# Kernel optimization log

Measured on AMD Instinct MI355X. Metric: run time of the kernel, lower is better.

## Reference

```python
import jax, jax.numpy as jnp
import numpy as np

D_MODEL = 512
NUM_HEADS = 8
D_K = D_MODEL // NUM_HEADS
SCALE = 1.0 / np.sqrt(D_K).astype(np.float32)


def _relative_shift(x):
    # x: (B, H, S, P) pos scores from Q @ P^T; Transformer-XL shift trick.
    b, h, s, p = x.shape
    x = jnp.pad(x, ((0, 0), (0, 0), (0, 0), (1, 0)))   # (B,H,S,P+1)
    x = x.reshape(b, h, p + 1, s)[:, :, 1:, :]          # drop first row
    x = x.reshape(b, h, s, p)[:, :, :, :s]
    return x


def setup_inputs() -> dict:
    key = jax.random.key(0)
    ks = jax.random.split(key, 10)
    B, S = 4, 2048
    glorot = lambda k: jax.random.uniform(
        k, (D_MODEL, D_MODEL), jnp.float32,
        -np.sqrt(6.0 / (2 * D_MODEL)), np.sqrt(6.0 / (2 * D_MODEL)))
    return {
        "inputs": jax.random.normal(ks[0], (B, S, D_MODEL), jnp.float32),
        "pos_enc": jax.random.normal(ks[1], (1, S, D_MODEL), jnp.float32),
        "W_q": glorot(ks[2]),
        "W_k": glorot(ks[3]),
        "W_v": glorot(ks[4]),
        "W_o": glorot(ks[5]),
        "W_pos": glorot(ks[6]),
        "u_bias": jnp.zeros((NUM_HEADS, D_K), jnp.float32),
        "v_bias": jnp.zeros((NUM_HEADS, D_K), jnp.float32),
    }


def reference(inputs, pos_enc, W_q, W_k, W_v, W_o, W_pos, u_bias, v_bias):
    B, S, _ = inputs.shape
    split = lambda x, b: x.reshape(b, S, NUM_HEADS, D_K).transpose(0, 2, 1, 3)
    Q = split(inputs @ W_q, B)        # (B,H,S,dk)
    K = split(inputs @ W_k, B)
    V = split(inputs @ W_v, B)
    P = split(pos_enc @ W_pos, 1)      # (1,H,S,dk)
    u = u_bias[None, :, None, :]
    v = v_bias[None, :, None, :]
    content_score = jnp.einsum('bhid,bhjd->bhij', Q + u, K)
    pos_score = jnp.einsum('bhid,xhjd->bhij', Q + v, P)  # broadcast over batch
    pos_score = _relative_shift(pos_score)
    scores = (content_score + pos_score) * SCALE
    attn = jax.nn.softmax(scores, axis=-1)  # no dropout (inference)
    context = jnp.einsum('bhij,bhjd->bhid', attn, V)
    context = context.transpose(0, 2, 1, 3).reshape(B, S, D_MODEL)
    return context @ W_o
```

## Files before the change

kernel.cpp:

```cpp
#include <hip/hip_runtime.h>
#include <hip/hip_bf16.h>
#include <math.h>

#define SEQ 2048
#define NH 8
#define DK 64
#define DM 512
#define QSCALE 0.18033688011112042f
#define PPAD (SEQ + 128)
#define POFF 64
#define KSTR 72
#define PSTR 36
#define ASTR 34

typedef unsigned short ushortT;
typedef short s16x8 __attribute__((ext_vector_type(8)));
typedef float f32x4 __attribute__((ext_vector_type(4)));

#define MFMA16 __builtin_amdgcn_mfma_f32_16x16x32_bf16

static __device__ __forceinline__ ushortT f2bf(float x) {
  __hip_bfloat16 h = __float2bfloat16(x);
  ushortT u;
  __builtin_memcpy(&u, &h, 2);
  return u;
}

static __device__ __forceinline__ float fexp2(float x) {
  return __builtin_amdgcn_exp2f(x);
}

static __device__ __forceinline__ s16x8 pack8(const float* p) {
  ushortT u[8];
#pragma unroll
  for (int i = 0; i < 8; ++i) u[i] = f2bf(p[i]);
  s16x8 out;
  __builtin_memcpy(&out, u, 16);
  return out;
}

static __device__ __forceinline__ int pinv(int j) {
  return (j < 16) ? ((j >> 2) * 8 + (j & 3)) : (((j >> 2) - 4) * 8 + 4 + (j & 3));
}

__global__ __launch_bounds__(256)
void cast_in(const float* __restrict__ X, const float* __restrict__ PE,
             ushortT* __restrict__ Xb, ushortT* __restrict__ PEb) {
  const size_t i4 = (size_t)blockIdx.x * 256 + threadIdx.x;
  const size_t NX = (size_t)4 * SEQ * DM / 4;
  const float4 v = (i4 < NX) ? *(const float4*)(X + i4 * 4)
                             : *(const float4*)(PE + (i4 - NX) * 4);
  ushortT o[4] = {f2bf(v.x), f2bf(v.y), f2bf(v.z), f2bf(v.w)};
  ushortT* dst = (i4 < NX) ? (Xb + i4 * 4) : (PEb + (i4 - NX) * 4);
  *(ulonglong1*)dst = *(ulonglong1*)o;
}

__global__ __launch_bounds__(256)
void transpose_w(const float* __restrict__ w0, const float* __restrict__ w1,
                 const float* __restrict__ w2, const float* __restrict__ w3,
                 const float* __restrict__ w4, ushortT* __restrict__ out) {
  __shared__ float ts[32][33];
  const int z = blockIdx.z;
  const float* w = (z == 0) ? w0 : (z == 1) ? w1 : (z == 2) ? w2 : (z == 3) ? w3 : w4;
  ushortT* o = out + (size_t)z * DM * DM;
  const int k0 = blockIdx.x * 32, n0 = blockIdx.y * 32;
  const int tx = threadIdx.x, ty = threadIdx.y;
#pragma unroll
  for (int i = 0; i < 4; ++i)
    ts[ty + i * 8][tx] = w[(size_t)(k0 + ty + i * 8) * DM + n0 + tx];
  __syncthreads();
#pragma unroll
  for (int i = 0; i < 4; ++i)
    o[(size_t)(n0 + ty + i * 8) * DM + k0 + tx] = f2bf(ts[tx][ty + i * 8]);
}

__global__ __launch_bounds__(256)
void gemm_mfma(const ushortT* __restrict__ A, const ushortT* __restrict__ Bt,
               const float* __restrict__ ubv, const float* __restrict__ vbv,
               ushortT* __restrict__ qu, ushortT* __restrict__ qv,
               ushortT* __restrict__ kb, ushortT* __restrict__ vt,
               float* __restrict__ of, int mode) {
  __shared__ ushortT As[128][ASTR];
  __shared__ ushortT Bs[128][ASTR];
  const int tid = threadIdx.x;
  const int w = tid >> 6, lane = tid & 63;
  const int c = lane & 15, q = lane >> 4;
  const int wm = w >> 1, wn = w & 1;
  const int m0 = blockIdx.x * 128, n0 = blockIdx.y * 128;
  const int lr = tid >> 1, lh = (tid & 1) * 16;

  f32x4 acc[4][4];
#pragma unroll
  for (int mt = 0; mt < 4; ++mt)
#pragma unroll
    for (int nt = 0; nt < 4; ++nt) acc[mt][nt] = (f32x4){0.f, 0.f, 0.f, 0.f};

  const ushortT* Ar = A + (size_t)(m0 + lr) * DM + lh;
  const ushortT* Br = Bt + (size_t)(n0 + lr) * DM + lh;
  uint4 a0 = *(const uint4*)(Ar);
  uint4 a1 = *(const uint4*)(Ar + 8);
  uint4 b0 = *(const uint4*)(Br);
  uint4 b1 = *(const uint4*)(Br + 8);

  for (int k0 = 0; k0 < DM; k0 += 32) {
    __syncthreads();
    *(uint4*)&As[lr][lh] = a0; *(uint4*)&As[lr][lh + 8] = a1;
    *(uint4*)&Bs[lr][lh] = b0; *(uint4*)&Bs[lr][lh + 8] = b1;
    __syncthreads();
    if (k0 + 32 < DM) {
      a0 = *(const uint4*)(Ar + k0 + 32);
      a1 = *(const uint4*)(Ar + k0 + 40);
      b0 = *(const uint4*)(Br + k0 + 32);
      b1 = *(const uint4*)(Br + k0 + 40);
    }
    s16x8 af[4], bf[4];
#pragma unroll
    for (int mt = 0; mt < 4; ++mt)
      af[mt] = *(const s16x8*)&As[wm * 64 + mt * 16 + c][q * 8];
#pragma unroll
    for (int nt = 0; nt < 4; ++nt)
      bf[nt] = *(const s16x8*)&Bs[wn * 64 + nt * 16 + c][q * 8];
#pragma unroll
    for (int mt = 0; mt < 4; ++mt)
#pragma unroll
      for (int nt = 0; nt < 4; ++nt)
        acc[mt][nt] = MFMA16(af[mt], bf[nt], acc[mt][nt], 0, 0, 0);
  }

#pragma unroll
  for (int mt = 0; mt < 4; ++mt)
#pragma unroll
    for (int nt = 0; nt < 4; ++nt)
#pragma unroll
      for (int r = 0; r < 4; ++r) {
        const int gm = m0 + wm * 64 + mt * 16 + q * 4 + r;
        const int gn = n0 + wn * 64 + nt * 16 + c;
        const float v = acc[mt][nt][r];
        const int bb = gm >> 11, s = gm & (SEQ - 1);
        if (mode == 0) {
          const int z = gn >> 9, gn5 = gn & 511;
          const int h = gn5 >> 6, d = gn5 & 63;
          if (z == 0) {
            const size_t base = (((size_t)bb * NH + h) * SEQ + s) * DK + d;
            qu[base] = f2bf((v + ubv[gn5]) * QSCALE);
            qv[base] = f2bf((v + vbv[gn5]) * QSCALE);
          } else if (z == 1) {
            kb[(((size_t)bb * NH + h) * SEQ + s) * DK + d] = f2bf(v);
          } else {
            const int s_il = (s & ~31) | pinv(s & 31);
            vt[(((size_t)bb * NH + h) * DK + d) * SEQ + s_il] = f2bf(v);
          }
        } else if (mode == 3) {
          const int h = gn >> 6, d = gn & 63;
          qu[((size_t)h * PPAD + POFF + gm) * DK + d] = f2bf(v);
        } else {
          of[(size_t)gm * DM + gn] = v;
        }
      }
}

static __device__ __forceinline__ f32x4 band_gemm(const ushortT* pb, int tile,
                                                  int c, int q, s16x8 a0, s16x8 a1) {
  const ushortT* pc = pb + (ptrdiff_t)(tile * 16 + c) * DK + q * 8;
  f32x4 G = {0.f, 0.f, 0.f, 0.f};
  G = MFMA16(a0, *(const s16x8*)pc, G, 0, 0, 0);
  G = MFMA16(a1, *(const s16x8*)(pc + 32), G, 0, 0, 0);
  return G;
}

static __device__ __forceinline__ f32x4 band_gemm_r(s16x8 a0, s16x8 a1,
                                                    s16x8 p0, s16x8 p1) {
  f32x4 G = {0.f, 0.f, 0.f, 0.f};
  G = MFMA16(a0, p0, G, 0, 0, 0);
  G = MFMA16(a1, p1, G, 0, 0, 0);
  return G;
}

static __device__ __forceinline__ void write_band2(float (*E)[PSTR], int c, int m_w,
                                                   f32x4 b0, f32x4 b1, f32x4 b2) {
#pragma unroll
  for (int r = 0; r < 4; ++r) {
    const int v = c + m_w + r - 15;
    const bool lo = (v >= 0);
    const int j1 = lo ? v : v + 16;
    const int p = ((j1 >> 2) << 3) | (j1 & 3);
    float* row = &E[m_w + r][p];
    row[0] = lo ? b0[r] : b1[r];
    row[4] = lo ? b1[r] : b2[r];
  }
}

__global__ __launch_bounds__(256, 3)
void attn_mfma(const ushortT* __restrict__ Qu, const ushortT* __restrict__ Qv,
               const ushortT* __restrict__ Kb, const ushortT* __restrict__ Vt,
               const ushortT* __restrict__ Pp, ushortT* __restrict__ ctxb) {
  const int n = blockIdx.x;
  const int xcd = n & 7, idx = n >> 3;
  const int b = idx >> 5, iblk = idx & 31;
  const int h = xcd, bh = b * 8 + h;
  const int tid = threadIdx.x;
  const int w = tid >> 6, lane = tid & 63;
  const int c = lane & 15, q = lane >> 4;
  const int i0 = iblk * 64;
  const int iw = i0 + w * 16;

  __shared__ ushortT Ks[64][KSTR];
  __shared__ ushortT Vs[64][KSTR];
  __shared__ float E1[4][2][16][PSTR];
  __shared__ float Lb[4][16];

  const ushortT* Qub = Qu + ((size_t)bh * SEQ + iw) * DK;
  const ushortT* Qvb = Qv + ((size_t)bh * SEQ + iw) * DK;
  const ushortT* Kbh = Kb + (size_t)bh * SEQ * DK;
  const ushortT* Vbh = Vt + (size_t)bh * DK * SEQ;
  const ushortT* Ph  = Pp + ((size_t)h * PPAD + POFF) * DK;

  const s16x8 qu0 = *(const s16x8*)(Qub + (size_t)c * DK + q * 8);
  const s16x8 qu1 = *(const s16x8*)(Qub + (size_t)c * DK + 32 + q * 8);
  const s16x8 qv0 = *(const s16x8*)(Qvb + (size_t)c * DK + q * 8);
  const s16x8 qv1 = *(const s16x8*)(Qvb + (size_t)c * DK + 32 + q * 8);
  const s16x8 qw0 = *(const s16x8*)(Qvb + (size_t)(c + 1) * DK + q * 8);
  const s16x8 qw1 = *(const s16x8*)(Qvb + (size_t)(c + 1) * DK + 32 + q * 8);

  int joff[8];
#pragma unroll
  for (int jj = 0; jj < 8; ++jj)
    joff[jj] = (jj < 4) ? (4 * q + jj) : (16 + 4 * q + (jj - 4));

  f32x4 O[4];
#pragma unroll
  for (int r = 0; r < 4; ++r) O[r] = (f32x4){0.f, 0.f, 0.f, 0.f};
  float lrow = 0.f;
  f32x4 e2c = (f32x4){0.f, 0.f, 0.f, 0.f};
  bool hv1 = false, hv2 = false;
  const int jt = iw & ~31;
  const int m_w = q * 4;

  {
    const ushortT* gk = Kbh;
    uint4 k0v = *(const uint4*)(gk + tid * 8);
    uint4 k1v = *(const uint4*)(gk + 2048 + tid * 8);
    const ushortT* gv = Vbh + (size_t)(tid >> 2) * SEQ + (tid & 3) * 16;
    uint4 v0v = *(const uint4*)gv;
    uint4 v1v = *(const uint4*)(gv + 8);
    *(uint4*)&Ks[tid >> 3][(tid & 7) * 8] = k0v;
    *(uint4*)&Ks[32 + (tid >> 3)][(tid & 7) * 8] = k1v;
    *(uint4*)&Vs[tid >> 2][(tid & 3) * 16] = v0v;
    *(uint4*)&Vs[tid >> 2][(tid & 3) * 16 + 8] = v1v;
  }
  __syncthreads();

  if (jt > 0) {
    const ushortT* pb1 = Ph + (ptrdiff_t)(0 - iw + SEQ - 16) * DK;
    f32x4 b0 = band_gemm(pb1, 0, c, q, qv0, qv1);
    f32x4 b1 = band_gemm(pb1, 1, c, q, qv0, qv1);
    e2c = band_gemm(pb1, 2, c, q, qv0, qv1);
    hv1 = true;
    write_band2(E1[w][0], c, m_w, b0, b1, e2c);
  }

#define PV_FROM(pr, jl)                                                       \
  {                                                                           \
    lrow += pr[0] + pr[1] + pr[2] + pr[3] + pr[4] + pr[5] + pr[6] + pr[7];    \
    const s16x8 pa = pack8(pr);                                               \
    _Pragma("unroll")                                                         \
    for (int dt = 0; dt < 4; ++dt) {                                          \
      const s16x8 vb = *(const s16x8*)&Vs[dt * 16 + c][(jl) + q * 8];         \
      O[dt] = MFMA16(pa, vb, O[dt], 0, 0, 0);                                 \
    }                                                                         \
  }

  for (int ch = 0; ch < 32; ++ch) {
    const bool more = (ch + 1) < 32;
    uint4 k0v, k1v, v0v, v1v;
    if (more) {
      const ushortT* gk = Kbh + (size_t)(ch + 1) * 64 * DK;
      k0v = *(const uint4*)(gk + tid * 8);
      k1v = *(const uint4*)(gk + 2048 + tid * 8);
      const ushortT* gv = Vbh + (size_t)(tid >> 2) * SEQ + (ch + 1) * 64 + (tid & 3) * 16;
      v0v = *(const uint4*)gv;
      v1v = *(const uint4*)(gv + 8);
    }
#pragma unroll
    for (int t = 0; t < 2; ++t) {
      const int nn = ch * 2 + t;
      const int j0 = nn * 32;
      const int jl = t * 32;
      const int drel = j0 - iw;
      const bool curB = (j0 >= jt) && (j0 < jt + 64);
      const int j0n = j0 + 32;
      const bool nxtB = (j0n >= jt) && (j0n < jt + 64);
      const bool haveNext = (nn + 1 < 64) && !nxtB;
      const bool nextA = (j0n < jt);

      const int dreln = j0n - iw;
      const int row1 = haveNext ? (nextA ? (dreln + SEQ - 16) : (dreln - 17)) : 0;
      const ushortT* pbn = Ph + (ptrdiff_t)row1 * DK;
      const ushortT* pc1 = pbn + (ptrdiff_t)(16 + c) * DK + q * 8;
      const ushortT* pc2 = pbn + (ptrdiff_t)(32 + c) * DK + q * 8;
      const s16x8 p10 = *(const s16x8*)pc1;
      const s16x8 p11 = *(const s16x8*)(pc1 + 32);
      const s16x8 p20 = *(const s16x8*)pc2;
      const s16x8 p21 = *(const s16x8*)(pc2 + 32);

      f32x4 S0 = {0.f, 0.f, 0.f, 0.f}, S1 = {0.f, 0.f, 0.f, 0.f};
      {
        const ushortT* ka = &Ks[jl + c][q * 8];
        S0 = MFMA16(*(const s16x8*)ka, qu0, S0, 0, 0, 0);
        S0 = MFMA16(*(const s16x8*)(ka + 32), qu1, S0, 0, 0, 0);
        const ushortT* ka2 = &Ks[jl + 16 + c][q * 8];
        S1 = MFMA16(*(const s16x8*)ka2, qu0, S1, 0, 0, 0);
        S1 = MFMA16(*(const s16x8*)(ka2 + 32), qu1, S1, 0, 0, 0);
      }

      if (curB) {
        {
          const ushortT* pb1 = Ph + (ptrdiff_t)(drel + SEQ - 16) * DK;
          f32x4 b0 = band_gemm(pb1, 0, c, q, qv0, qv1);
          f32x4 b1 = band_gemm(pb1, 1, c, q, qv0, qv1);
          f32x4 b2 = band_gemm(pb1, 2, c, q, qv0, qv1);
          write_band2(E1[w][nn & 1], c, m_w, b0, b1, b2);
        }
        {
          const ushortT* pb2 = Ph + (ptrdiff_t)(drel - 17) * DK;
          f32x4 b0 = band_gemm(pb2, 0, c, q, qw0, qw1);
          f32x4 b1 = band_gemm(pb2, 1, c, q, qw0, qw1);
          f32x4 b2 = band_gemm(pb2, 2, c, q, qw0, qw1);
          write_band2(E1[w][(nn + 1) & 1], c, m_w, b0, b1, b2);
        }
        const float* e1r = &E1[w][nn & 1][c][q * 8];
        const float* e2r = &E1[w][(nn + 1) & 1][c][q * 8];
        float4 aA = *(const float4*)e1r, aB = *(const float4*)(e1r + 4);
        float4 bA = *(const float4*)e2r, bB = *(const float4*)(e2r + 4);
        float f1[8] = {aA.x, aA.y, aA.z, aA.w, aB.x, aB.y, aB.z, aB.w};
        float f2[8] = {bA.x, bA.y, bA.z, bA.w, bB.x, bB.y, bB.z, bB.w};
        float sv[8] = {S0[0], S0[1], S0[2], S0[3], S1[0], S1[1], S1[2], S1[3]};
        float pr[8];
#pragma unroll
        for (int jj = 0; jj < 8; ++jj) {
          const int dlt = drel + joff[jj] - c;
          const float g = (dlt <= 0) ? f1[jj] : ((dlt == 1) ? 0.0f : f2[jj]);
          pr[jj] = fexp2(sv[jj] + g);
        }
        PV_FROM(pr, jl)
      } else {
        const float* e1r = &E1[w][nn & 1][c][q * 8];
        float4 fA = *(const float4*)e1r, fB = *(const float4*)(e1r + 4);
        float pr[8] = {fexp2(S0[0] + fA.x), fexp2(S0[1] + fA.y),
                       fexp2(S0[2] + fA.z), fexp2(S0[3] + fA.w),
                       fexp2(S1[0] + fB.x), fexp2(S1[1] + fB.y),
                       fexp2(S1[2] + fB.z), fexp2(S1[3] + fB.w)};
        PV_FROM(pr, jl)
      }

      if (haveNext) {
        f32x4 b0, b1, b2;
        if (nextA) {
          if (hv1) b0 = e2c;
          else { b0 = band_gemm(pbn, 0, c, q, qv0, qv1); hv1 = true; }
          b1 = band_gemm_r(qv0, qv1, p10, p11);
          b2 = band_gemm_r(qv0, qv1, p20, p21);
        } else {
          if (hv2) b0 = e2c;
          else { b0 = band_gemm(pbn, 0, c, q, qw0, qw1); hv2 = true; }
          b1 = band_gemm_r(qw0, qw1, p10, p11);
          b2 = band_gemm_r(qw0, qw1, p20, p21);
        }
        e2c = b2;
        write_band2(E1[w][(nn + 1) & 1], c, m_w, b0, b1, b2);
      }
    }
    __syncthreads();
    if (more) {
      *(uint4*)&Ks[tid >> 3][(tid & 7) * 8] = k0v;
      *(uint4*)&Ks[32 + (tid >> 3)][(tid & 7) * 8] = k1v;
      *(uint4*)&Vs[tid >> 2][(tid & 3) * 16] = v0v;
      *(uint4*)&Vs[tid >> 2][(tid & 3) * 16 + 8] = v1v;
    }
    __syncthreads();
  }

  lrow += __shfl_xor(lrow, 16);
  lrow += __shfl_xor(lrow, 32);
  if (q == 0) Lb[w][c] = lrow;
  float inv[4];
#pragma unroll
  for (int r = 0; r < 4; ++r) inv[r] = 1.0f / Lb[w][q * 4 + r];
#pragma unroll
  for (int dt = 0; dt < 4; ++dt)
#pragma unroll
    for (int r = 0; r < 4; ++r) {
      const int i = iw + q * 4 + r;
      ctxb[((size_t)b * SEQ + i) * DM + h * DK + dt * 16 + c] = f2bf(O[dt][r] * inv[r]);
    }
}

extern "C" void kernel_launch(void* const* d_in, const int* in_sizes, int n_in,
                              void* d_out, int out_size, void* d_ws, size_t ws_size,
                              hipStream_t stream) {
  (void)in_sizes; (void)n_in; (void)out_size; (void)ws_size;
  const float* X   = (const float*)d_in[0];
  const float* PE  = (const float*)d_in[1];
  const float* Wq  = (const float*)d_in[2];
  const float* Wk  = (const float*)d_in[3];
  const float* Wv  = (const float*)d_in[4];
  const float* Wo  = (const float*)d_in[5];
  const float* Wp  = (const float*)d_in[6];
  const float* ubv = (const float*)d_in[7];
  const float* vbv = (const float*)d_in[8];

  const size_t NX = (size_t)4 * SEQ * DM;
  const size_t NP = (size_t)SEQ * DM;
  const size_t NW = (size_t)DM * DM;
  ushortT* Xb  = (ushortT*)d_ws;
  ushortT* PEb = Xb + NX;
  ushortT* Wt  = PEb + NP;
  ushortT* qu  = Wt + 5 * NW;
  ushortT* qv  = qu + NX;
  ushortT* kb  = qv + NX;
  ushortT* vt  = kb + NX;
  ushortT* pp  = vt + NX;
  ushortT* ctx = pp + (size_t)NH * PPAD * DK;
  float* outp = (float*)d_out;

  hipLaunchKernelGGL(cast_in, dim3((NX + NP) / 4 / 256), dim3(256), 0, stream, X, PE, Xb, PEb);
  hipLaunchKernelGGL(transpose_w, dim3(16, 16, 5), dim3(32, 8), 0, stream, Wq, Wk, Wv, Wp, Wo, Wt);
  dim3 blk(256);
  hipLaunchKernelGGL(gemm_mfma, dim3(64, 12), blk, 0, stream, Xb, Wt, ubv, vbv,
                     qu, qv, kb, vt, (float*)nullptr, 0);
  hipLaunchKernelGGL(gemm_mfma, dim3(16, 4), blk, 0, stream, PEb, Wt + 3 * NW, ubv, vbv,
                     pp, (ushortT*)nullptr, (ushortT*)nullptr, (ushortT*)nullptr, (float*)nullptr, 3);
  hipLaunchKernelGGL(attn_mfma, dim3(1024), blk, 0, stream, qu, qv, kb, vt, pp, ctx);
  hipLaunchKernelGGL(gemm_mfma, dim3(64, 4), blk, 0, stream, ctx, Wt + 4 * NW, ubv, vbv,
                     (ushortT*)nullptr, (ushortT*)nullptr, (ushortT*)nullptr, (ushortT*)nullptr, outp, 4);
}
```

Before: 373.8 us.

## Software-pipeline softmax exp and PV MFMA one tile behind QK scores

Defers the exp and P·V MFMA for each non-band 32-column tile to the next iteration, carrying the score, bias and V fragments in registers. The current tile's QK^T MFMAs can then overlap the previous tile's exp and PV work, hiding MFMA latency. K and V fragments are loaded from LDS up front. The cost is more live registers, which may lower occupancy or cause spills, and one extra combine step after the loop.

```diff
diff --git a/kernel.cpp b/kernel.cpp
--- a/kernel.cpp
+++ b/kernel.cpp
@@ -236,6 +236,11 @@
   const int jt = iw & ~31;
   const int m_w = q * 4;
 
+  f32x4 Sp0, Sp1;
+  float4 fEpA, fEpB;
+  s16x8 vbp0, vbp1, vbp2, vbp3;
+  bool have_prev = false;
+
   {
     const ushortT* gk = Kbh;
     uint4 k0v = *(const uint4*)(gk + tid * 8);
@@ -259,15 +264,18 @@
     write_band2(E1[w][0], c, m_w, b0, b1, e2c);
   }
 
-#define PV_FROM(pr, jl)                                                       \
-  {                                                                           \
+#define DEF_COMBINE()                                                         \
+  if (have_prev) {                                                            \
+    float pr[8] = {fexp2(Sp0[0] + fEpA.x), fexp2(Sp0[1] + fEpA.y),            \
+                   fexp2(Sp0[2] + fEpA.z), fexp2(Sp0[3] + fEpA.w),            \
+                   fexp2(Sp1[0] + fEpB.x), fexp2(Sp1[1] + fEpB.y),            \
+                   fexp2(Sp1[2] + fEpB.z), fexp2(Sp1[3] + fEpB.w)};           \
     lrow += pr[0] + pr[1] + pr[2] + pr[3] + pr[4] + pr[5] + pr[6] + pr[7];    \
     const s16x8 pa = pack8(pr);                                               \
-    _Pragma("unroll")                                                         \
-    for (int dt = 0; dt < 4; ++dt) {                                          \
-      const s16x8 vb = *(const s16x8*)&Vs[dt * 16 + c][(jl) + q * 8];         \
-      O[dt] = MFMA16(pa, vb, O[dt], 0, 0, 0);                                 \
-    }                                                                         \
+    O[0] = MFMA16(pa, vbp0, O[0], 0, 0, 0);                                   \
+    O[1] = MFMA16(pa, vbp1, O[1], 0, 0, 0);                                   \
+    O[2] = MFMA16(pa, vbp2, O[2], 0, 0, 0);                                   \
+    O[3] = MFMA16(pa, vbp3, O[3], 0, 0, 0);                                   \
   }
 
   for (int ch = 0; ch < 32; ++ch) {
@@ -303,15 +311,32 @@
       const s16x8 p20 = *(const s16x8*)pc2;
       const s16x8 p21 = *(const s16x8*)(pc2 + 32);
 
-      f32x4 S0 = {0.f, 0.f, 0.f, 0.f}, S1 = {0.f, 0.f, 0.f, 0.f};
-      {
-        const ushortT* ka = &Ks[jl + c][q * 8];
-        S0 = MFMA16(*(const s16x8*)ka, qu0, S0, 0, 0, 0);
-        S0 = MFMA16(*(const s16x8*)(ka + 32), qu1, S0, 0, 0, 0);
-        const ushortT* ka2 = &Ks[jl + 16 + c][q * 8];
-        S1 = MFMA16(*(const s16x8*)ka2, qu0, S1, 0, 0, 0);
-        S1 = MFMA16(*(const s16x8*)(ka2 + 32), qu1, S1, 0, 0, 0);
+      const ushortT* ka = &Ks[jl + c][q * 8];
+      const s16x8 kf0 = *(const s16x8*)ka;
+      const s16x8 kf1 = *(const s16x8*)(ka + 32);
+      const ushortT* ka2 = &Ks[jl + 16 + c][q * 8];
+      const s16x8 kf2 = *(const s16x8*)ka2;
+      const s16x8 kf3 = *(const s16x8*)(ka2 + 32);
+      const s16x8 vc0 = *(const s16x8*)&Vs[0 * 16 + c][jl + q * 8];
+      const s16x8 vc1 = *(const s16x8*)&Vs[1 * 16 + c][jl + q * 8];
+      const s16x8 vc2 = *(const s16x8*)&Vs[2 * 16 + c][jl + q * 8];
+      const s16x8 vc3 = *(const s16x8*)&Vs[3 * 16 + c][jl + q * 8];
+
+      f32x4 T0 = {0.f, 0.f, 0.f, 0.f}, T1 = {0.f, 0.f, 0.f, 0.f};
+      T0 = MFMA16(kf0, qu0, T0, 0, 0, 0);
+      T0 = MFMA16(kf1, qu1, T0, 0, 0, 0);
+      T1 = MFMA16(kf2, qu0, T1, 0, 0, 0);
+      T1 = MFMA16(kf3, qu1, T1, 0, 0, 0);
+
+      float4 gA = {0.f, 0.f, 0.f, 0.f}, gB = {0.f, 0.f, 0.f, 0.f};
+      if (!curB) {
+        const float* e1r = &E1[w][nn & 1][c][q * 8];
+        gA = *(const float4*)e1r;
+        gB = *(const float4*)(e1r + 4);
       }
+
+      DEF_COMBINE()
+      have_prev = false;
 
       if (curB) {
         {
@@ -334,7 +359,7 @@
         float4 bA = *(const float4*)e2r, bB = *(const float4*)(e2r + 4);
         float f1[8] = {aA.x, aA.y, aA.z, aA.w, aB.x, aB.y, aB.z, aB.w};
         float f2[8] = {bA.x, bA.y, bA.z, bA.w, bB.x, bB.y, bB.z, bB.w};
-        float sv[8] = {S0[0], S0[1], S0[2], S0[3], S1[0], S1[1], S1[2], S1[3]};
+        float sv[8] = {T0[0], T0[1], T0[2], T0[3], T1[0], T1[1], T1[2], T1[3]};
         float pr[8];
 #pragma unroll
         for (int jj = 0; jj < 8; ++jj) {
@@ -342,15 +367,17 @@
           const float g = (dlt <= 0) ? f1[jj] : ((dlt == 1) ? 0.0f : f2[jj]);
           pr[jj] = fexp2(sv[jj] + g);
         }
-        PV_FROM(pr, jl)
+        lrow += pr[0] + pr[1] + pr[2] + pr[3] + pr[4] + pr[5] + pr[6] + pr[7];
+        const s16x8 pa = pack8(pr);
+        O[0] = MFMA16(pa, vc0, O[0], 0, 0, 0);
+        O[1] = MFMA16(pa, vc1, O[1], 0, 0, 0);
+        O[2] = MFMA16(pa, vc2, O[2], 0, 0, 0);
+        O[3] = MFMA16(pa, vc3, O[3], 0, 0, 0);
       } else {
-        const float* e1r = &E1[w][nn & 1][c][q * 8];
-        float4 fA = *(const float4*)e1r, fB = *(const float4*)(e1r + 4);
-        float pr[8] = {fexp2(S0[0] + fA.x), fexp2(S0[1] + fA.y),
-                       fexp2(S0[2] + fA.z), fexp2(S0[3] + fA.w),
-                       fexp2(S1[0] + fB.x), fexp2(S1[1] + fB.y),
-                       fexp2(S1[2] + fB.z), fexp2(S1[3] + fB.w)};
-        PV_FROM(pr, jl)
+        Sp0 = T0; Sp1 = T1;
+        fEpA = gA; fEpB = gB;
+        vbp0 = vc0; vbp1 = vc1; vbp2 = vc2; vbp3 = vc3;
+        have_prev = true;
       }
 
       if (haveNext) {
@@ -380,6 +407,8 @@
     __syncthreads();
   }
 
+  DEF_COMBINE()
+
   lrow += __shfl_xor(lrow, 16);
   lrow += __shfl_xor(lrow, 32);
   if (q == 0) Lb[w][c] = lrow;
```

After: 527.8 us. 41.2% more time.
